# Optimization experiments

Hardware: AMD Instinct MI355X
Metric: run time of the kernel (lower is better)

## Reference

```python
import jax, jax.numpy as jnp
import numpy as np

NEG_SLOPE = 0.2  # init arg negative_slope


def setup_inputs() -> dict:
    key = jax.random.key(0)
    k1, k2, k3, k4 = jax.random.split(key, 4)
    N, E, D_IN, D_OUT = 8192, 262144, 128, 128
    h = jax.random.normal(k1, (N, D_IN), dtype=jnp.float32)
    edge_index = jax.random.randint(k2, (2, E), 0, N, dtype=jnp.int64)
    # nn.Linear(in, out, bias=False) weight: [out, in]
    W = jax.random.normal(k3, (D_OUT, D_IN), dtype=jnp.float32) * (1.0 / np.sqrt(D_IN))
    # att parameter: [2*out, 1], xavier-uniform-ish scale
    lim = np.sqrt(6.0 / (2 * D_OUT + 1)) * 1.414
    att = jax.random.uniform(k4, (2 * D_OUT, 1), dtype=jnp.float32, minval=-lim, maxval=lim)
    return {"h": h, "edge_index": edge_index, "W": W, "att": att}


def reference(h, edge_index, W, att):
    # h: [N, d_in], edge_index: [2, E], W: [d_out, d_in], att: [2*d_out, 1]
    h_trans = h @ W.T                                  # [N, d_out]
    row, col = edge_index[0], edge_index[1]
    e = jnp.concatenate([h_trans[row], h_trans[col]], axis=1)  # [E, 2*d_out]
    edge_e = jnp.squeeze(e @ att, axis=-1)             # [E]
    edge_e = jnp.where(edge_e >= 0, edge_e, NEG_SLOPE * edge_e)  # leaky_relu
    N = h.shape[0]
    attention = jnp.zeros((N, N), dtype=h_trans.dtype).at[row, col].set(edge_e)
    attention = (attention + attention.T) * 0.5        # symmetrize
    fill_value = edge_e.max()                          # .item() -> constant (no grad)
    diag = jnp.arange(N)
    attention = attention.at[diag, diag].set(fill_value)
    attention = jax.nn.softmax(attention, axis=1)      # row softmax over dense NxN
    h_prime = attention @ h_trans                      # [N, d_out]
    h_prime = jax.nn.elu(h_prime)                      # concat=True -> ELU
    # F.dropout in eval mode is identity
    return h_prime, attention
```

## Files before the change

### kernel.cpp

```cpp
#include <hip/hip_runtime.h>
#include <stdint.h>

#define NN 8192
#define EE 262144
#define DD 128
#define NEGS 0.2f
#define HBITS 20
#define HSIZE (1<<HBITS)
#define HMASK (HSIZE-1)
#define BCAP 192

typedef float f32x4 __attribute__((ext_vector_type(4)));

__device__ __forceinline__ unsigned f2ord(float f){
  unsigned u = __float_as_uint(f);
  return (u & 0x80000000u) ? ~u : (u | 0x80000000u);
}
__device__ __forceinline__ float ord2f(unsigned u){
  return __uint_as_float((u & 0x80000000u) ? (u & 0x7fffffffu) : ~u);
}
__device__ __forceinline__ unsigned hmix(int key){
  unsigned h = (unsigned)key * 2654435761u;
  h ^= h >> 15;
  return h;
}

__global__ void k_setup(int* hkeys, int* hvals, int* cnt, float* T,
                        unsigned* fillmax, const float* __restrict__ W,
                        float* __restrict__ wt){
  int gid = blockIdx.x*256 + threadIdx.x;
  int4 m1 = {-1,-1,-1,-1};
  if(gid < HSIZE/4)            ((int4*)hkeys)[gid] = m1;
  else if(gid < HSIZE/2)       ((int4*)hvals)[gid - HSIZE/4] = m1;
  if(gid < NN/4)               ((int4*)cnt)[gid] = int4{0,0,0,0};
  if(gid < DD/4)               ((float4*)T)[gid] = float4{0.f,0.f,0.f,0.f};
  if(gid == 0)                 *fillmax = 0x007FFFFFu;
  if(gid < DD*DD){
    int c = gid >> 7, k = gid & 127;
    wt[k*DD + c] = W[gid];
  }
}

__global__ __launch_bounds__(256) void k_gemm(const float* __restrict__ h,
                                              const float* __restrict__ wt,
                                              float* __restrict__ ht){
  __shared__ float wl[64*DD];
  __shared__ float hl[16][132];
  int t = threadIdx.x;
  int row0 = blockIdx.x * 16;
  #pragma unroll
  for(int u=0;u<2;u++){
    int f4 = u*256 + t;
    int r = f4 >> 5, k4 = f4 & 31;
    float4 v = ((const float4*)(h + (size_t)(row0+r)*DD))[k4];
    *((float4*)&hl[r][k4*4]) = v;
  }
  int r  = t & 15;
  int c0 = (t >> 4) * 8;
  float acc[8];
  #pragma unroll
  for(int s=0;s<8;s++) acc[s]=0.f;
  for(int p=0;p<2;p++){
    __syncthreads();
    const float4* wsrc = (const float4*)(wt + p*64*DD);
    float4* wd = (float4*)wl;
    #pragma unroll
    for(int u=0;u<8;u++) wd[u*256+t] = wsrc[u*256+t];
    __syncthreads();
    #pragma unroll 2
    for(int kk=0;kk<64;kk++){
      float hv = hl[r][p*64+kk];
      const float4* wr4 = (const float4*)&wl[kk*DD + c0];
      float4 w0 = wr4[0], w1 = wr4[1];
      acc[0] += hv*w0.x; acc[1] += hv*w0.y; acc[2] += hv*w0.z; acc[3] += hv*w0.w;
      acc[4] += hv*w1.x; acc[5] += hv*w1.y; acc[6] += hv*w1.z; acc[7] += hv*w1.w;
    }
  }
  float4* o = (float4*)(ht + (size_t)(row0+r)*DD + c0);
  o[0] = float4{acc[0],acc[1],acc[2],acc[3]};
  o[1] = float4{acc[4],acc[5],acc[6],acc[7]};
}

__global__ __launch_bounds__(256) void k_stats(const float* __restrict__ ht,
    const float* __restrict__ att, float* T, float* a1, float* a2){
  int t = threadIdx.x, b = blockIdx.x;
  int lane = t & 63;
  int i = b*4 + (t >> 6);
  const float* hr = ht + (size_t)i*DD;
  float h0 = hr[lane], h1 = hr[lane+64];
  float x1 = h0*att[lane]    + h1*att[lane+64];
  float x2 = h0*att[DD+lane] + h1*att[DD+lane+64];
  #pragma unroll
  for(int o=32;o>0;o>>=1){ x1 += __shfl_down(x1,o); x2 += __shfl_down(x2,o); }
  if(lane==0){ a1[i]=x1; a2[i]=x2; }
  if(b < 64){
    __shared__ float part[256];
    int c = t & 127, half = t >> 7;
    float s = 0.f;
    int r0 = b*128 + half*64;
    for(int rr=r0; rr<r0+64; rr++) s += ht[(size_t)rr*DD + c];
    part[t] = s; __syncthreads();
    if(half==0) atomicAdd(&T[c], part[t] + part[t+128]);
  }
}

__global__ void k_edge(const int* __restrict__ ei, const float* __restrict__ a1,
                       const float* __restrict__ a2, float* __restrict__ val,
                       unsigned* fillmax, int* hkeys, int* hvals){
  int k = blockIdx.x*256 + threadIdx.x;
  int r = ei[k], c = ei[EE + k];
  float e = a1[r] + a2[c];
  e = e >= 0.f ? e : NEGS*e;
  val[k] = e;
  float wm = e;
  #pragma unroll
  for(int o=32;o>0;o>>=1) wm = fmaxf(wm, __shfl_down(wm,o));
  __shared__ float sm[4];
  if((threadIdx.x & 63)==0) sm[threadIdx.x>>6] = wm;
  __syncthreads();
  if(threadIdx.x==0){
    float bm = fmaxf(fmaxf(sm[0],sm[1]), fmaxf(sm[2],sm[3]));
    atomicMax(fillmax, f2ord(bm));
  }
  if(r != c){
    int key = (r<<13) | c;
    unsigned slot = hmix(key) & HMASK;
    while(true){
      int prev = atomicCAS(&hkeys[slot], -1, key);
      if(prev == -1 || prev == key){ atomicMax(&hvals[slot], k); break; }
      slot = (slot + 1) & HMASK;
    }
  }
}

__global__ void k_fill(const int* __restrict__ hkeys, const int* __restrict__ hvals,
                       const float* __restrict__ val, int* cnt,
                       int2* __restrict__ bucket){
  int base = (blockIdx.x*256 + threadIdx.x) * 2;
  #pragma unroll
  for(int u=0;u<2;u++){
    int s = base + u;
    int key = hkeys[s];
    if(key < 0) continue;
    int i = key >> 13, j = key & (NN-1);
    int kwin = hvals[s];
    int rkey = (j<<13) | i;
    unsigned slot = hmix(rkey) & HMASK;
    int krev = -1;
    while(true){
      int kk = hkeys[slot];
      if(kk == rkey){ krev = hvals[slot]; break; }
      if(kk == -1) break;
      slot = (slot + 1) & HMASK;
    }
    float a = 0.5f * (val[kwin] + (krev >= 0 ? val[krev] : 0.f));
    int p = atomicAdd(&cnt[i], 1);
    if(p < BCAP) bucket[(size_t)i*BCAP + p] = int2{j, __float_as_int(a)};
    if(krev < 0){
      int q = atomicAdd(&cnt[j], 1);
      if(q < BCAP) bucket[(size_t)j*BCAP + q] = int2{i, __float_as_int(a)};
    }
  }
}

__global__ __launch_bounds__(256) void k_out(const float* __restrict__ ht,
    const float* __restrict__ T, const int* __restrict__ cnt,
    const int2* __restrict__ bucket, const unsigned* __restrict__ fillmax,
    float* __restrict__ hprime, float* __restrict__ attn){
  __shared__ float rowbuf[NN];
  __shared__ float red[16];
  __shared__ float hacc[2][DD];
  int i = blockIdx.x, t = threadIdx.x;
  int lane = t & 63, w = t >> 6;
  float fill = ord2f(*fillmax);
  int n = min(cnt[i], BCAP);
  const int2* brow = bucket + (size_t)i*BCAP;
  float mx = -INFINITY;
  for(int e=t; e<n; e+=256) mx = fmaxf(mx, __int_as_float(brow[e].y));
  #pragma unroll
  for(int o=32;o>0;o>>=1) mx = fmaxf(mx, __shfl_xor(mx,o));
  if(lane==0) red[w] = mx;
  __syncthreads();
  mx = fmaxf(fmaxf(red[0],red[1]), fmaxf(red[2],red[3]));
  float m = fmaxf(fill, mx);
  m = fmaxf(m, 0.f);
  float ds = 0.f;
  for(int e=t; e<n; e+=256) ds += __expf(__int_as_float(brow[e].y) - m);
  #pragma unroll
  for(int o=32;o>0;o>>=1) ds += __shfl_xor(ds,o);
  if(lane==0) red[8+w] = ds;
  __syncthreads();
  ds = red[8]+red[9]+red[10]+red[11];
  float ez = __expf(-m);
  float ef = __expf(fill - m);
  float denom = ds + ef + (float)(NN-1-n)*ez;
  float invd = 1.f/denom;
  int d = t & 127, half = t >> 7;
  float acc = (half==0) ? (ez*T[d] + (ef-ez)*ht[(size_t)i*DD+d]) : 0.f;
  for(int e=half; e<n; e+=2){
    int2 be = brow[e];
    float wgt = __expf(__int_as_float(be.y) - m) - ez;
    acc += wgt * ht[(size_t)be.x*DD + d];
  }
  hacc[half][d] = acc;
  __syncthreads();
  if(t < DD){
    float s = (hacc[0][t] + hacc[1][t]) * invd;
    s = s > 0.f ? s : expm1f(s);
    hprime[(size_t)i*DD + t] = s;
  }
  float z = ez*invd;
  float4 zv = {z,z,z,z};
  float4* rb4 = (float4*)rowbuf;
  #pragma unroll
  for(int u=0;u<8;u++) rb4[u*256+t] = zv;
  __syncthreads();
  for(int e=t; e<n; e+=256){
    int2 be = brow[e];
    rowbuf[be.x] = __expf(__int_as_float(be.y)-m)*invd;
  }
  if(t==0) rowbuf[i] = ef*invd;
  __syncthreads();
  const f32x4* rbn = (const f32x4*)rowbuf;
  f32x4* o = (f32x4*)(attn + (size_t)i*NN);
  #pragma unroll
  for(int u=0;u<8;u++) __builtin_nontemporal_store(rbn[u*256+t], o + u*256+t);
}

extern "C" void kernel_launch(void* const* d_in, const int* in_sizes, int n_in,
                              void* d_out, int out_size, void* d_ws, size_t ws_size,
                              hipStream_t stream){
  const float* h   = (const float*)d_in[0];
  const int*   ei  = (const int*)d_in[1];
  const float* W   = (const float*)d_in[2];
  const float* att = (const float*)d_in[3];
  float* out = (float*)d_out;
  float* hprime = out;
  float* attn   = out + (size_t)NN*DD;

  int*   hkeys = (int*)attn;
  int*   hvals = hkeys + HSIZE;
  float* val   = (float*)(hvals + HSIZE);
  float* a1    = val + EE;
  float* a2    = a1 + NN;

  char* ws = (char*)d_ws;
  size_t off = 0;
  auto alloc = [&](size_t bytes)->char*{
    char* p = ws + off;
    off = (off + bytes + 255) & ~(size_t)255;
    return p;
  };
  float* ht      = (float*)alloc((size_t)NN*DD*4);
  float* wt      = (float*)alloc((size_t)DD*DD*4);
  float* T       = (float*)alloc((size_t)DD*4);
  int*   cnt     = (int*)alloc((size_t)NN*4);
  unsigned* fillmax = (unsigned*)alloc(256);
  int2*  bucket  = (int2*)alloc((size_t)NN*BCAP*8);

  k_setup <<<2048, 256, 0, stream>>>(hkeys, hvals, cnt, T, fillmax, W, wt);
  k_gemm  <<<NN/16, 256, 0, stream>>>(h, wt, ht);
  k_stats <<<NN/4, 256, 0, stream>>>(ht, att, T, a1, a2);
  k_edge  <<<EE/256, 256, 0, stream>>>(ei, a1, a2, val, fillmax, hkeys, hvals);
  k_fill  <<<HSIZE/512, 256, 0, stream>>>(hkeys, hvals, val, cnt, bucket);
  k_out   <<<NN, 256, 0, stream>>>(ht, T, cnt, bucket, fillmax, hprime, attn);
}
```

Before: 235.4 us.

## Split output kernel into row-stats, dense z-fill and sparse scatter patch

The monolithic per-row output kernel is replaced by three kernels. The first computes softmax statistics and h_prime with one wavefront per row, dropping the max pass because fill already bounds every edge value. The second is a purely streaming kernel that writes the constant off-edge value across the whole dense attention matrix. The third scatters the edge and diagonal entries. This removes the 32KB per-block LDS row buffer, which limited occupancy, and makes the large dense write a simple bandwidth-bound stream. The cost is extra launches and random scattered writes into attention after the fill. Bucket capacity also grows to 256 so rows can be indexed with a shift.

```diff
diff --git a/kernel.cpp b/kernel.cpp
--- a/kernel.cpp
+++ b/kernel.cpp
@@ -8,7 +8,7 @@
 #define HBITS 20
 #define HSIZE (1<<HBITS)
 #define HMASK (HSIZE-1)
-#define BCAP 192
+#define BCAP 256
 
 typedef float f32x4 __attribute__((ext_vector_type(4)));
 
@@ -155,76 +155,77 @@
     }
     float a = 0.5f * (val[kwin] + (krev >= 0 ? val[krev] : 0.f));
     int p = atomicAdd(&cnt[i], 1);
-    if(p < BCAP) bucket[(size_t)i*BCAP + p] = int2{j, __float_as_int(a)};
+    if(p < BCAP) bucket[((size_t)i<<8) + p] = int2{j, __float_as_int(a)};
     if(krev < 0){
       int q = atomicAdd(&cnt[j], 1);
-      if(q < BCAP) bucket[(size_t)j*BCAP + q] = int2{i, __float_as_int(a)};
-    }
-  }
-}
-
-__global__ __launch_bounds__(256) void k_out(const float* __restrict__ ht,
+      if(q < BCAP) bucket[((size_t)j<<8) + q] = int2{i, __float_as_int(a)};
+    }
+  }
+}
+
+__global__ __launch_bounds__(256) void k_rowstats(const float* __restrict__ ht,
     const float* __restrict__ T, const int* __restrict__ cnt,
     const int2* __restrict__ bucket, const unsigned* __restrict__ fillmax,
-    float* __restrict__ hprime, float* __restrict__ attn){
-  __shared__ float rowbuf[NN];
-  __shared__ float red[16];
-  __shared__ float hacc[2][DD];
-  int i = blockIdx.x, t = threadIdx.x;
-  int lane = t & 63, w = t >> 6;
+    float* inv_, float* z_, float* dg_, float* __restrict__ hprime){
+  int lane = threadIdx.x & 63;
+  int i = blockIdx.x*4 + (threadIdx.x >> 6);
   float fill = ord2f(*fillmax);
+  float m = fmaxf(fill, 0.f);
   int n = min(cnt[i], BCAP);
-  const int2* brow = bucket + (size_t)i*BCAP;
-  float mx = -INFINITY;
-  for(int e=t; e<n; e+=256) mx = fmaxf(mx, __int_as_float(brow[e].y));
-  #pragma unroll
-  for(int o=32;o>0;o>>=1) mx = fmaxf(mx, __shfl_xor(mx,o));
-  if(lane==0) red[w] = mx;
-  __syncthreads();
-  mx = fmaxf(fmaxf(red[0],red[1]), fmaxf(red[2],red[3]));
-  float m = fmaxf(fill, mx);
-  m = fmaxf(m, 0.f);
+  const int2* brow = bucket + ((size_t)i<<8);
   float ds = 0.f;
-  for(int e=t; e<n; e+=256) ds += __expf(__int_as_float(brow[e].y) - m);
+  for(int e=lane; e<n; e+=64) ds += __expf(__int_as_float(brow[e].y) - m);
   #pragma unroll
   for(int o=32;o>0;o>>=1) ds += __shfl_xor(ds,o);
-  if(lane==0) red[8+w] = ds;
-  __syncthreads();
-  ds = red[8]+red[9]+red[10]+red[11];
   float ez = __expf(-m);
   float ef = __expf(fill - m);
   float denom = ds + ef + (float)(NN-1-n)*ez;
   float invd = 1.f/denom;
-  int d = t & 127, half = t >> 7;
-  float acc = (half==0) ? (ez*T[d] + (ef-ez)*ht[(size_t)i*DD+d]) : 0.f;
-  for(int e=half; e<n; e+=2){
+  if(lane==0){ inv_[i]=invd; z_[i]=ez*invd; dg_[i]=ef*invd; }
+  const float* hti = ht + (size_t)i*DD;
+  float acc0 = ez*T[lane]    + (ef-ez)*hti[lane];
+  float acc1 = ez*T[lane+64] + (ef-ez)*hti[lane+64];
+  for(int e=0;e<n;e++){
     int2 be = brow[e];
-    float wgt = __expf(__int_as_float(be.y) - m) - ez;
-    acc += wgt * ht[(size_t)be.x*DD + d];
-  }
-  hacc[half][d] = acc;
-  __syncthreads();
-  if(t < DD){
-    float s = (hacc[0][t] + hacc[1][t]) * invd;
-    s = s > 0.f ? s : expm1f(s);
-    hprime[(size_t)i*DD + t] = s;
-  }
-  float z = ez*invd;
-  float4 zv = {z,z,z,z};
-  float4* rb4 = (float4*)rowbuf;
-  #pragma unroll
-  for(int u=0;u<8;u++) rb4[u*256+t] = zv;
-  __syncthreads();
-  for(int e=t; e<n; e+=256){
-    int2 be = brow[e];
-    rowbuf[be.x] = __expf(__int_as_float(be.y)-m)*invd;
-  }
-  if(t==0) rowbuf[i] = ef*invd;
-  __syncthreads();
-  const f32x4* rbn = (const f32x4*)rowbuf;
-  f32x4* o = (f32x4*)(attn + (size_t)i*NN);
-  #pragma unroll
-  for(int u=0;u<8;u++) __builtin_nontemporal_store(rbn[u*256+t], o + u*256+t);
+    float w = __expf(__int_as_float(be.y) - m) - ez;
+    const float* htj = ht + (size_t)be.x*DD;
+    acc0 += w*htj[lane];
+    acc1 += w*htj[lane+64];
+  }
+  acc0 *= invd; acc1 *= invd;
+  acc0 = acc0 > 0.f ? acc0 : expm1f(acc0);
+  acc1 = acc1 > 0.f ? acc1 : expm1f(acc1);
+  hprime[(size_t)i*DD + lane]      = acc0;
+  hprime[(size_t)i*DD + lane + 64] = acc1;
+}
+
+__global__ __launch_bounds__(256) void k_zfill(const float* __restrict__ z_,
+                                               float* __restrict__ attn){
+  int idx = blockIdx.x*256 + threadIdx.x;
+  f32x4* o = (f32x4*)attn;
+  #pragma unroll
+  for(int u=0;u<16;u++){
+    int f4i = idx + u*(4096*256);
+    float z = z_[f4i >> 11];
+    f32x4 v = {z,z,z,z};
+    __builtin_nontemporal_store(v, o + f4i);
+  }
+}
+
+__global__ void k_patch(const int* __restrict__ cnt, const int2* __restrict__ bucket,
+                        const unsigned* __restrict__ fillmax,
+                        const float* __restrict__ inv_, const float* __restrict__ dg_,
+                        float* __restrict__ attn){
+  int s = blockIdx.x*256 + threadIdx.x;
+  int i = s >> 8, e = s & 255;
+  float fill = ord2f(*fillmax);
+  float m = fmaxf(fill, 0.f);
+  int n = min(cnt[i], BCAP);
+  if(e < n){
+    int2 be = bucket[s];
+    attn[((size_t)i<<13) + be.x] = __expf(__int_as_float(be.y) - m) * inv_[i];
+  }
+  if(s < NN) attn[((size_t)s<<13) + s] = dg_[s];
 }
 
 extern "C" void kernel_launch(void* const* d_in, const int* in_sizes, int n_in,
@@ -255,13 +256,18 @@
   float* wt      = (float*)alloc((size_t)DD*DD*4);
   float* T       = (float*)alloc((size_t)DD*4);
   int*   cnt     = (int*)alloc((size_t)NN*4);
+  float* inv_    = (float*)alloc((size_t)NN*4);
+  float* z_      = (float*)alloc((size_t)NN*4);
+  float* dg_     = (float*)alloc((size_t)NN*4);
   unsigned* fillmax = (unsigned*)alloc(256);
   int2*  bucket  = (int2*)alloc((size_t)NN*BCAP*8);
 
-  k_setup <<<2048, 256, 0, stream>>>(hkeys, hvals, cnt, T, fillmax, W, wt);
-  k_gemm  <<<NN/16, 256, 0, stream>>>(h, wt, ht);
-  k_stats <<<NN/4, 256, 0, stream>>>(ht, att, T, a1, a2);
-  k_edge  <<<EE/256, 256, 0, stream>>>(ei, a1, a2, val, fillmax, hkeys, hvals);
-  k_fill  <<<HSIZE/512, 256, 0, stream>>>(hkeys, hvals, val, cnt, bucket);
-  k_out   <<<NN, 256, 0, stream>>>(ht, T, cnt, bucket, fillmax, hprime, attn);
-}
+  k_setup   <<<2048, 256, 0, stream>>>(hkeys, hvals, cnt, T, fillmax, W, wt);
+  k_gemm    <<<NN/16, 256, 0, stream>>>(h, wt, ht);
+  k_stats   <<<NN/4, 256, 0, stream>>>(ht, att, T, a1, a2);
+  k_edge    <<<EE/256, 256, 0, stream>>>(ei, a1, a2, val, fillmax, hkeys, hvals);
+  k_fill    <<<HSIZE/512, 256, 0, stream>>>(hkeys, hvals, val, cnt, bucket);
+  k_rowstats<<<NN/4, 256, 0, stream>>>(ht, T, cnt, bucket, fillmax, inv_, z_, dg_, hprime);
+  k_zfill   <<<4096, 256, 0, stream>>>(z_, attn);
+  k_patch   <<<NN*BCAP/256, 256, 0, stream>>>(cnt, bucket, fillmax, inv_, dg_, attn);
+}
```

After: 231.9 us. Within noise of the previous version (-1.5%).
